# Performance work log

Hardware: AMD Instinct MI355X
Metric: run time of the kernel (lower is better)

Reference implementation:

```python
import jax, jax.numpy as jnp
import numpy as np

DIM = 768
NUM_HEADS = 12
HEAD_DIM = DIM // NUM_HEADS  # 64


def setup_inputs() -> dict:
    key = jax.random.key(0)
    k1, k2, k3, k4 = jax.random.split(key, 4)
    B, N = 2, 2048
    x = jax.random.normal(k1, (B, N, DIM), dtype=jnp.float32)
    att_mask = jnp.ones((B, N), dtype=jnp.int32)
    # learned params (qkv has no bias since qkv_bias=False)
    qkv_w = jax.random.normal(k2, (3 * DIM, DIM), dtype=jnp.float32) * (1.0 / np.sqrt(DIM))
    proj_w = jax.random.normal(k3, (DIM, DIM), dtype=jnp.float32) * (1.0 / np.sqrt(DIM))
    proj_b = jax.random.normal(k4, (DIM,), dtype=jnp.float32) * 0.02
    return {"x": x, "att_mask": att_mask, "qkv_w": qkv_w, "proj_w": proj_w, "proj_b": proj_b}


def reference(x, att_mask, qkv_w, proj_w, proj_b):
    B, N, C = x.shape
    H, Dh = NUM_HEADS, HEAD_DIM
    scale = Dh ** (-0.5)
    # qkv projection: [B,N,3C] -> [3,B,H,N,Dh]
    qkv = jnp.einsum('bnc,oc->bno', x, qkv_w)
    qkv = qkv.reshape(B, N, 3, H, Dh).transpose(2, 0, 3, 1, 4)
    q, k, v = qkv[0], qkv[1], qkv[2]
    q = q * scale
    # full N x N logits (the memory-bound hotspot)
    logit = jnp.einsum('bhnd,bhmd->bhnm', q, k)
    # 2D mask path: [B,N] -> [B,1,1,N], masked_fill(mask==0, -inf)
    mask = att_mask[:, None, None, :]
    logit = jnp.where(mask == 0, -jnp.inf, logit)
    attn = jax.nn.softmax(logit, axis=-1)  # attn_drop is identity (p=0, eval)
    out = jnp.einsum('bhnm,bhmd->bhnd', attn, v)
    out = out.transpose(0, 2, 1, 3).reshape(B, N, H * Dh)
    out = jnp.einsum('bnc,oc->bno', out, proj_w) + proj_b  # proj_drop identity
    return out
```

## Files before the change

### kernel.cpp

```cpp
#include <hip/hip_runtime.h>
#include <hip/hip_bf16.h>
#include <math.h>
#include <cstdint>
#include <cstddef>

typedef __bf16 bf16x8 __attribute__((ext_vector_type(8)));
typedef float  f32x4  __attribute__((ext_vector_type(4)));

#define GLOAD16(g, l) __builtin_amdgcn_global_load_lds( \
    (const __attribute__((address_space(1))) void*)(g),  \
    (__attribute__((address_space(3))) void*)(l), 16, 0, 0)

__device__ __forceinline__ unsigned short f2bf(float f) {
    union { float f; unsigned u; } v; v.f = f;
    unsigned u = v.u;
    u += 0x7fffu + ((u >> 16) & 1u);
    return (unsigned short)(u >> 16);
}

__device__ __forceinline__ unsigned pack_bf16x2(float a, float b) {
    __hip_bfloat162 h = __float22bfloat162_rn(make_float2(a, b));
    return *reinterpret_cast<unsigned*>(&h);
}

__global__ __launch_bounds__(256) void cvt_all(
    const float* __restrict__ x,
    const float* __restrict__ qkvw,
    const float* __restrict__ projw,
    unsigned short* __restrict__ xb,
    unsigned short* __restrict__ wqkv,
    unsigned short* __restrict__ wproj)
{
    const int N1 = 4096 * 768;
    const int N2 = 2304 * 768;
    const int SC = 768 * 768;
    const float C2 = 0.18033688011112042f;
    int i = ((int)blockIdx.x * 256 + (int)threadIdx.x) * 4;

    const float* src;
    unsigned short* dst;
    int j;
    bool sc = false;
    if (i < N1)           { src = x;     dst = xb;    j = i; }
    else if (i < N1 + N2) { j = i - N1;  src = qkvw;  dst = wqkv;  sc = (j < SC); }
    else                  { j = i - N1 - N2; src = projw; dst = wproj; }

    float4 v = *reinterpret_cast<const float4*>(src + j);
    if (sc) { v.x *= C2; v.y *= C2; v.z *= C2; v.w *= C2; }
    uint2 pk;
    pk.x = pack_bf16x2(v.x, v.y);
    pk.y = pack_bf16x2(v.z, v.w);
    *reinterpret_cast<uint2*>(dst + j) = pk;
}

template <int MODE, int MROWS, int NF>
__global__ __launch_bounds__(256) void gemm_bt(
    const unsigned short* __restrict__ A,
    const unsigned short* __restrict__ B,
    unsigned short* __restrict__ Cb,
    unsigned short* __restrict__ Vt,
    float* __restrict__ Cf,
    const float* __restrict__ bias,
    int M, int N, int K)
{
    constexpr int MI = MROWS / 32;
    __shared__ __align__(16) unsigned short Al[2][MROWS * 64];
    __shared__ __align__(16) unsigned short Bl[2][NF * 32 * 64];
    const int bm   = blockIdx.x * MROWS;
    const int bn   = blockIdx.y * (NF * 32);
    const int tid  = (int)threadIdx.x;
    const int wave = tid >> 6;
    const int lane = tid & 63;
    const int wr   = wave >> 1;
    const int wc   = wave & 1;
    const int q    = lane & 15;
    const int g4   = (lane >> 4) * 4;

    f32x4 acc[MI][NF] = {};

    const int srow = lane >> 3;
    const int scol = (lane & 7) * 8;

    auto stage = [&](int buf, int k0) {
#pragma unroll
        for (int i = 0; i < MI; ++i) {
            const int chunk = wave * MI + i;
            GLOAD16(A + (size_t)(bm + chunk * 8 + srow) * K + (k0 + scol),
                    &Al[buf][chunk * 512]);
        }
#pragma unroll
        for (int i = 0; i < NF; ++i) {
            const int chunk = wave * NF + i;
            GLOAD16(B + (size_t)(bn + chunk * 8 + srow) * K + (k0 + scol),
                    &Bl[buf][chunk * 512]);
        }
    };

    stage(0, 0);
    __syncthreads();

    const int nt = K / 64;
    int buf = 0;
    for (int t = 0; t < nt; ++t) {
        if (t + 1 < nt) stage(buf ^ 1, (t + 1) * 64);
#pragma unroll
        for (int kk = 0; kk < 2; ++kk) {
            const int ko = kk * 32 + (lane >> 4) * 8;
            bf16x8 af[MI], bf[NF];
#pragma unroll
            for (int mi = 0; mi < MI; ++mi)
                af[mi] = *(const bf16x8*)&Al[buf][(wr * (MROWS / 2) + mi * 16 + q) * 64 + ko];
#pragma unroll
            for (int ni = 0; ni < NF; ++ni)
                bf[ni] = *(const bf16x8*)&Bl[buf][(wc * 16 * NF + ni * 16 + q) * 64 + ko];
#pragma unroll
            for (int mi = 0; mi < MI; ++mi)
#pragma unroll
                for (int ni = 0; ni < NF; ++ni)
                    acc[mi][ni] = __builtin_amdgcn_mfma_f32_16x16x32_bf16(
                        af[mi], bf[ni], acc[mi][ni], 0, 0, 0);
        }
        __syncthreads();
        buf ^= 1;
    }

#pragma unroll
    for (int mi = 0; mi < MI; ++mi) {
        const int row0 = bm + wr * (MROWS / 2) + mi * 16 + g4;
        if constexpr (MODE == 1) {
#pragma unroll
            for (int ni = 0; ni < NF; ++ni) {
                const int col = bn + wc * 16 * NF + ni * 16 + q;
#pragma unroll
                for (int r = 0; r < 4; ++r)
                    Cf[(size_t)(row0 + r) * N + col] = acc[mi][ni][r] + bias[col];
            }
        } else {
            if (bn < 1536) {
#pragma unroll
                for (int ni = 0; ni < NF; ++ni) {
                    const int col = bn + wc * 16 * NF + ni * 16 + q;
#pragma unroll
                    for (int r = 0; r < 4; ++r)
                        Cb[(size_t)(row0 + r) * 1536 + col] = f2bf(acc[mi][ni][r]);
                }
            } else {
                const int b  = row0 >> 11;
                const int np = row0 & 2047;
#pragma unroll
                for (int ni = 0; ni < NF; ++ni) {
                    const int vcol = bn + wc * 16 * NF + ni * 16 + q - 1536;
                    const int hv = vcol >> 6, d = vcol & 63;
                    uint2 w;
                    w.x = pack_bf16x2(acc[mi][ni][0], acc[mi][ni][1]);
                    w.y = pack_bf16x2(acc[mi][ni][2], acc[mi][ni][3]);
                    *reinterpret_cast<uint2*>(
                        &Vt[((size_t)(b * 12 + hv) * 64 + d) * 2048 + np]) = w;
                }
            }
        }
    }
}

__global__ __launch_bounds__(256, 4) void attn_fwd(
    const unsigned short* __restrict__ qk,
    const unsigned short* __restrict__ vT,
    const int* __restrict__ mask,
    unsigned short* __restrict__ out)
{
    const int NN = 2048, H = 12;
    const int bh = (int)blockIdx.y;
    const int b  = bh / H, h = bh % H;
    const int q0 = (int)blockIdx.x * 64;
    const int tid = (int)threadIdx.x, wave = tid >> 6, lane = tid & 63;
    const int g   = lane >> 4;
    const int q   = lane & 15;
    const int swz = (lane & 7) << 3;

    __shared__ __align__(16) unsigned short Kl[2][64 * 64];
    __shared__ __align__(16) unsigned short Vl[2][64 * 64];
    __shared__ __align__(16) unsigned short Pl[4][16 * 64];

    bool allone;
    {
        const int* mrow = mask + b * NN + lane * 32;
        unsigned mv = 0xFFFFFFFFu;
#pragma unroll
        for (int i = 0; i < 8; ++i) {
            int4 m = *reinterpret_cast<const int4*>(mrow + i * 4);
            mv = min(mv, min(min((unsigned)m.x, (unsigned)m.y),
                             min((unsigned)m.z, (unsigned)m.w)));
        }
        allone = __all(mv != 0u);
    }

    const size_t qrow = (size_t)(b * NN + q0 + wave * 16 + q) * 1536 + h * 64;
    bf16x8 qf[2];
    qf[0] = *reinterpret_cast<const bf16x8*>(&qk[qrow + g * 8]);
    qf[1] = *reinterpret_cast<const bf16x8*>(&qk[qrow + 32 + g * 8]);

    const int srcc = ((lane & 7) ^ (lane >> 3)) * 8;
    const int srow = lane >> 3;
    const char* kg0 = (const char*)(qk + (size_t)(b * NN + wave * 16 + srow) * 1536 + 768 + h * 64 + srcc);
    const char* kg1 = kg0 + (size_t)8 * 1536 * 2;
    const char* vg0 = (const char*)(vT + (size_t)(bh * 64 + wave * 16 + srow) * 2048 + srcc);
    const char* vg1 = vg0 + (size_t)8 * 2048 * 2;

    auto stageK = [&](int buf) {
        GLOAD16(kg0, &Kl[buf][wave * 1024]);
        GLOAD16(kg1, &Kl[buf][wave * 1024 + 512]);
        kg0 += (size_t)64 * 1536 * 2;
        kg1 += (size_t)64 * 1536 * 2;
    };
    auto stageV = [&](int buf) {
        GLOAD16(vg0, &Vl[buf][wave * 1024]);
        GLOAD16(vg1, &Vl[buf][wave * 1024 + 512]);
        vg0 += 128;
        vg1 += 128;
    };

    f32x4 oacc[4] = {};
    float l_i = 0.f;

    stageK(0); stageV(0);
    asm volatile("s_waitcnt vmcnt(0)\n\ts_barrier" ::: "memory");

    int cur = 0;
    for (int it = 0; it < 32; ++it) {
        if (it < 31) { stageV(cur ^ 1); stageK(cur ^ 1); }

        f32x4 s[4] = {};
        __builtin_amdgcn_s_setprio(1);
#pragma unroll
        for (int kk = 0; kk < 2; ++kk) {
            const int ko = kk * 32 + g * 8;
#pragma unroll
            for (int ni = 0; ni < 4; ++ni) {
                bf16x8 kf = *(const bf16x8*)&Kl[cur][(16 * ni + q) * 64 + (ko ^ swz)];
                s[ni] = __builtin_amdgcn_mfma_f32_16x16x32_bf16(kf, qf[kk], s[ni], 0, 0, 0);
            }
        }
        __builtin_amdgcn_s_setprio(0);

        if (!allone) {
#pragma unroll
            for (int ni = 0; ni < 4; ++ni) {
                int4 mr = *reinterpret_cast<const int4*>(
                    &mask[b * NN + it * 64 + 16 * ni + 4 * g]);
                if (mr.x == 0) s[ni][0] = -INFINITY;
                if (mr.y == 0) s[ni][1] = -INFINITY;
                if (mr.z == 0) s[ni][2] = -INFINITY;
                if (mr.w == 0) s[ni][3] = -INFINITY;
            }
        }

        float p[4][4];
#pragma unroll
        for (int ni = 0; ni < 4; ++ni)
#pragma unroll
            for (int r = 0; r < 4; ++r)
                p[ni][r] = __builtin_amdgcn_exp2f(s[ni][r]);
        float rs0 = (p[0][0] + p[0][1]) + (p[0][2] + p[0][3]);
        float rs1 = (p[1][0] + p[1][1]) + (p[1][2] + p[1][3]);
        float rs2 = (p[2][0] + p[2][1]) + (p[2][2] + p[2][3]);
        float rs3 = (p[3][0] + p[3][1]) + (p[3][2] + p[3][3]);
        l_i += (rs0 + rs1) + (rs2 + rs3);

#pragma unroll
        for (int ni = 0; ni < 4; ++ni) {
            uint2 pw;
            pw.x = pack_bf16x2(p[ni][0], p[ni][1]);
            pw.y = pack_bf16x2(p[ni][2], p[ni][3]);
            const int kvb = 16 * ni + 4 * g;
            *reinterpret_cast<uint2*>(&Pl[wave][q * 64 + (kvb ^ ((q & 7) << 3))]) = pw;
        }

        __builtin_amdgcn_s_setprio(1);
#pragma unroll
        for (int kk = 0; kk < 2; ++kk) {
            const int ko = kk * 32 + g * 8;
            bf16x8 pf = *(const bf16x8*)&Pl[wave][q * 64 + (ko ^ ((q & 7) << 3))];
#pragma unroll
            for (int ct = 0; ct < 4; ++ct) {
                bf16x8 vf = *(const bf16x8*)&Vl[cur][(16 * ct + q) * 64 + (ko ^ swz)];
                oacc[ct] = __builtin_amdgcn_mfma_f32_16x16x32_bf16(vf, pf, oacc[ct], 0, 0, 0);
            }
        }
        __builtin_amdgcn_s_setprio(0);

        asm volatile("s_waitcnt vmcnt(0)\n\ts_barrier" ::: "memory");
        cur ^= 1;
    }

    l_i += __shfl_xor(l_i, 16);
    l_i += __shfl_xor(l_i, 32);
    const float inv = 1.0f / l_i;
    const size_t orow = (size_t)(b * NN + q0 + wave * 16 + q) * 768 + h * 64;
#pragma unroll
    for (int ct = 0; ct < 4; ++ct) {
        uint2 ow;
        ow.x = pack_bf16x2(oacc[ct][0] * inv, oacc[ct][1] * inv);
        ow.y = pack_bf16x2(oacc[ct][2] * inv, oacc[ct][3] * inv);
        *reinterpret_cast<uint2*>(&out[orow + 16 * ct + 4 * g]) = ow;
    }
}

extern "C" void kernel_launch(void* const* d_in, const int* in_sizes, int n_in,
                              void* d_out, int out_size, void* d_ws, size_t ws_size,
                              hipStream_t stream)
{
    const float* x      = (const float*)d_in[0];
    const int*   mask   = (const int*)d_in[1];
    const float* qkv_w  = (const float*)d_in[2];
    const float* proj_w = (const float*)d_in[3];
    const float* proj_b = (const float*)d_in[4];
    float* out = (float*)d_out;

    const int BN = 2 * 2048;
    const int C  = 768;
    const int C3 = 2304;

    char* w = (char*)d_ws;
    unsigned short* xb    = (unsigned short*)w; w += (size_t)BN * C    * 2;
    unsigned short* wqkv  = (unsigned short*)w; w += (size_t)C3 * C    * 2;
    unsigned short* wproj = (unsigned short*)w; w += (size_t)C  * C    * 2;
    unsigned short* qk    = (unsigned short*)w; w += (size_t)BN * 1536 * 2;
    unsigned short* vT    = (unsigned short*)w; w += (size_t)24 * 64 * 2048 * 2;
    unsigned short* ao    = (unsigned short*)w;

    {
        const int total = (BN * C + C3 * C + C * C) / 4;
        cvt_all<<<total / 256, 256, 0, stream>>>(x, qkv_w, proj_w, xb, wqkv, wproj);
    }

    gemm_bt<2, 128, 4><<<dim3(BN / 128, C3 / 128), 256, 0, stream>>>(
        xb, wqkv, qk, vT, nullptr, nullptr, BN, C3, C);

    attn_fwd<<<dim3(2048 / 64, 24), 256, 0, stream>>>(qk, vT, mask, ao);

    gemm_bt<1, 64, 2><<<dim3(BN / 64, C / 64), 256, 0, stream>>>(
        ao, wproj, nullptr, nullptr, out, proj_b, BN, C, C);
}
```

Before: 109.1 us.

## Split attention KV tile across waves and reduce partial outputs via LDS

The attention kernel now gives each wave a 16-key slice of each KV tile for all 64 queries, instead of a 16-query slice over all keys. Probabilities stay in registers and feed 16x16x16 MFMAs directly, which removes the per-wave P round-trip through LDS. Each wave keeps a 4x4 accumulator grid and per-query row sums, so partial outputs and sums from the four waves are combined through LDS at the end. The costs are more VGPRs (occupancy bound lowered from 4 to 3), a tree reduction with extra barriers, and twice as many smaller MFMAs in the PV step.

```diff
diff --git a/kernel.cpp b/kernel.cpp
--- a/kernel.cpp
+++ b/kernel.cpp
@@ -5,6 +5,8 @@
 #include <cstddef>
 
 typedef __bf16 bf16x8 __attribute__((ext_vector_type(8)));
+typedef __bf16 bf16x4 __attribute__((ext_vector_type(4)));
+typedef short  s16x4  __attribute__((ext_vector_type(4)));
 typedef float  f32x4  __attribute__((ext_vector_type(4)));
 
 #define GLOAD16(g, l) __builtin_amdgcn_global_load_lds( \
@@ -21,6 +23,19 @@
 __device__ __forceinline__ unsigned pack_bf16x2(float a, float b) {
     __hip_bfloat162 h = __float22bfloat162_rn(make_float2(a, b));
     return *reinterpret_cast<unsigned*>(&h);
+}
+
+__device__ __forceinline__ f32x4 mfma16(bf16x4 a, bf16x4 b, f32x4 c) {
+#if __has_builtin(__builtin_amdgcn_mfma_f32_16x16x16_bf16)
+    return __builtin_amdgcn_mfma_f32_16x16x16_bf16(a, b, c, 0, 0, 0);
+#elif __has_builtin(__builtin_amdgcn_mfma_f32_16x16x16bf16_1k)
+    return __builtin_amdgcn_mfma_f32_16x16x16bf16_1k(
+        __builtin_bit_cast(s16x4, a), __builtin_bit_cast(s16x4, b), c, 0, 0, 0);
+#else
+    asm volatile("v_mfma_f32_16x16x16_bf16 %0, %1, %2, %0"
+                 : "+v"(c) : "v"(a), "v"(b));
+    return c;
+#endif
 }
 
 __global__ __launch_bounds__(256) void cvt_all(
@@ -162,7 +177,7 @@
     }
 }
 
-__global__ __launch_bounds__(256, 4) void attn_fwd(
+__global__ __launch_bounds__(256, 3) void attn_fwd(
     const unsigned short* __restrict__ qk,
     const unsigned short* __restrict__ vT,
     const int* __restrict__ mask,
@@ -175,11 +190,11 @@
     const int tid = (int)threadIdx.x, wave = tid >> 6, lane = tid & 63;
     const int g   = lane >> 4;
     const int q   = lane & 15;
-    const int swz = (lane & 7) << 3;
-
-    __shared__ __align__(16) unsigned short Kl[2][64 * 64];
-    __shared__ __align__(16) unsigned short Vl[2][64 * 64];
-    __shared__ __align__(16) unsigned short Pl[4][16 * 64];
+    const int swz = (q & 7) << 3;
+
+    __shared__ __align__(16) unsigned short LDS[16896];
+    unsigned short* Kl0 = LDS;
+    unsigned short* Vl0 = LDS + 8192;
 
     bool allone;
     {
@@ -194,10 +209,13 @@
         allone = __all(mv != 0u);
     }
 
-    const size_t qrow = (size_t)(b * NN + q0 + wave * 16 + q) * 1536 + h * 64;
-    bf16x8 qf[2];
-    qf[0] = *reinterpret_cast<const bf16x8*>(&qk[qrow + g * 8]);
-    qf[1] = *reinterpret_cast<const bf16x8*>(&qk[qrow + 32 + g * 8]);
+    bf16x8 qf[2][4];
+#pragma unroll
+    for (int kk = 0; kk < 2; ++kk)
+#pragma unroll
+        for (int qt = 0; qt < 4; ++qt)
+            qf[kk][qt] = *reinterpret_cast<const bf16x8*>(
+                &qk[(size_t)(b * NN + q0 + 16 * qt + q) * 1536 + h * 64 + kk * 32 + g * 8]);
 
     const int srcc = ((lane & 7) ^ (lane >> 3)) * 8;
     const int srow = lane >> 3;
@@ -207,20 +225,20 @@
     const char* vg1 = vg0 + (size_t)8 * 2048 * 2;
 
     auto stageK = [&](int buf) {
-        GLOAD16(kg0, &Kl[buf][wave * 1024]);
-        GLOAD16(kg1, &Kl[buf][wave * 1024 + 512]);
+        GLOAD16(kg0, &Kl0[buf * 4096 + wave * 1024]);
+        GLOAD16(kg1, &Kl0[buf * 4096 + wave * 1024 + 512]);
         kg0 += (size_t)64 * 1536 * 2;
         kg1 += (size_t)64 * 1536 * 2;
     };
     auto stageV = [&](int buf) {
-        GLOAD16(vg0, &Vl[buf][wave * 1024]);
-        GLOAD16(vg1, &Vl[buf][wave * 1024 + 512]);
+        GLOAD16(vg0, &Vl0[buf * 4096 + wave * 1024]);
+        GLOAD16(vg1, &Vl0[buf * 4096 + wave * 1024 + 512]);
         vg0 += 128;
         vg1 += 128;
     };
 
-    f32x4 oacc[4] = {};
-    float l_i = 0.f;
+    f32x4 oacc[4][4] = {};
+    float l[4] = {0.f, 0.f, 0.f, 0.f};
 
     stageK(0); stageV(0);
     asm volatile("s_waitcnt vmcnt(0)\n\ts_barrier" ::: "memory");
@@ -233,58 +251,48 @@
         __builtin_amdgcn_s_setprio(1);
 #pragma unroll
         for (int kk = 0; kk < 2; ++kk) {
-            const int ko = kk * 32 + g * 8;
-#pragma unroll
-            for (int ni = 0; ni < 4; ++ni) {
-                bf16x8 kf = *(const bf16x8*)&Kl[cur][(16 * ni + q) * 64 + (ko ^ swz)];
-                s[ni] = __builtin_amdgcn_mfma_f32_16x16x32_bf16(kf, qf[kk], s[ni], 0, 0, 0);
+            bf16x8 kf = *(const bf16x8*)&Kl0[cur * 4096 + (16 * wave + q) * 64
+                                             + ((kk * 32 + g * 8) ^ swz)];
+#pragma unroll
+            for (int qt = 0; qt < 4; ++qt)
+                s[qt] = __builtin_amdgcn_mfma_f32_16x16x32_bf16(kf, qf[kk][qt], s[qt], 0, 0, 0);
+        }
+        __builtin_amdgcn_s_setprio(0);
+
+        if (!allone) {
+            int4 mr = *reinterpret_cast<const int4*>(
+                &mask[b * NN + it * 64 + 16 * wave + 4 * g]);
+#pragma unroll
+            for (int qt = 0; qt < 4; ++qt) {
+                if (mr.x == 0) s[qt][0] = -INFINITY;
+                if (mr.y == 0) s[qt][1] = -INFINITY;
+                if (mr.z == 0) s[qt][2] = -INFINITY;
+                if (mr.w == 0) s[qt][3] = -INFINITY;
             }
         }
-        __builtin_amdgcn_s_setprio(0);
-
-        if (!allone) {
-#pragma unroll
-            for (int ni = 0; ni < 4; ++ni) {
-                int4 mr = *reinterpret_cast<const int4*>(
-                    &mask[b * NN + it * 64 + 16 * ni + 4 * g]);
-                if (mr.x == 0) s[ni][0] = -INFINITY;
-                if (mr.y == 0) s[ni][1] = -INFINITY;
-                if (mr.z == 0) s[ni][2] = -INFINITY;
-                if (mr.w == 0) s[ni][3] = -INFINITY;
-            }
-        }
-
-        float p[4][4];
-#pragma unroll
-        for (int ni = 0; ni < 4; ++ni)
-#pragma unroll
-            for (int r = 0; r < 4; ++r)
-                p[ni][r] = __builtin_amdgcn_exp2f(s[ni][r]);
-        float rs0 = (p[0][0] + p[0][1]) + (p[0][2] + p[0][3]);
-        float rs1 = (p[1][0] + p[1][1]) + (p[1][2] + p[1][3]);
-        float rs2 = (p[2][0] + p[2][1]) + (p[2][2] + p[2][3]);
-        float rs3 = (p[3][0] + p[3][1]) + (p[3][2] + p[3][3]);
-        l_i += (rs0 + rs1) + (rs2 + rs3);
-
-#pragma unroll
-        for (int ni = 0; ni < 4; ++ni) {
-            uint2 pw;
-            pw.x = pack_bf16x2(p[ni][0], p[ni][1]);
-            pw.y = pack_bf16x2(p[ni][2], p[ni][3]);
-            const int kvb = 16 * ni + 4 * g;
-            *reinterpret_cast<uint2*>(&Pl[wave][q * 64 + (kvb ^ ((q & 7) << 3))]) = pw;
+
+        bf16x4 pb[4];
+#pragma unroll
+        for (int qt = 0; qt < 4; ++qt) {
+            float p0 = __builtin_amdgcn_exp2f(s[qt][0]);
+            float p1 = __builtin_amdgcn_exp2f(s[qt][1]);
+            float p2 = __builtin_amdgcn_exp2f(s[qt][2]);
+            float p3 = __builtin_amdgcn_exp2f(s[qt][3]);
+            l[qt] += (p0 + p1) + (p2 + p3);
+            uint2 t;
+            t.x = pack_bf16x2(p0, p1);
+            t.y = pack_bf16x2(p2, p3);
+            pb[qt] = __builtin_bit_cast(bf16x4, t);
         }
 
         __builtin_amdgcn_s_setprio(1);
 #pragma unroll
-        for (int kk = 0; kk < 2; ++kk) {
-            const int ko = kk * 32 + g * 8;
-            bf16x8 pf = *(const bf16x8*)&Pl[wave][q * 64 + (ko ^ ((q & 7) << 3))];
-#pragma unroll
-            for (int ct = 0; ct < 4; ++ct) {
-                bf16x8 vf = *(const bf16x8*)&Vl[cur][(16 * ct + q) * 64 + (ko ^ swz)];
-                oacc[ct] = __builtin_amdgcn_mfma_f32_16x16x32_bf16(vf, pf, oacc[ct], 0, 0, 0);
-            }
+        for (int ct = 0; ct < 4; ++ct) {
+            bf16x4 va = *(const bf16x4*)&Vl0[cur * 4096 + (16 * ct + q) * 64
+                                             + ((16 * wave + 4 * g) ^ swz)];
+#pragma unroll
+            for (int qt = 0; qt < 4; ++qt)
+                oacc[ct][qt] = mfma16(va, pb[qt], oacc[ct][qt]);
         }
         __builtin_amdgcn_s_setprio(0);
 
@@ -292,16 +300,61 @@
         cur ^= 1;
     }
 
-    l_i += __shfl_xor(l_i, 16);
-    l_i += __shfl_xor(l_i, 32);
-    const float inv = 1.0f / l_i;
-    const size_t orow = (size_t)(b * NN + q0 + wave * 16 + q) * 768 + h * 64;
-#pragma unroll
-    for (int ct = 0; ct < 4; ++ct) {
-        uint2 ow;
-        ow.x = pack_bf16x2(oacc[ct][0] * inv, oacc[ct][1] * inv);
-        ow.y = pack_bf16x2(oacc[ct][2] * inv, oacc[ct][3] * inv);
-        *reinterpret_cast<uint2*>(&out[orow + 16 * ct + 4 * g]) = ow;
+#pragma unroll
+    for (int qt = 0; qt < 4; ++qt) {
+        l[qt] += __shfl_xor(l[qt], 16);
+        l[qt] += __shfl_xor(l[qt], 32);
+    }
+    float* lb = (float*)&LDS[16384];
+    float* fb = (float*)&LDS[0];
+    if (g == 0) {
+#pragma unroll
+        for (int qt = 0; qt < 4; ++qt) lb[wave * 64 + qt * 16 + q] = l[qt];
+    }
+    if (wave & 1) {
+        float* dst = fb + (wave >> 1) * 4096;
+#pragma unroll
+        for (int ct = 0; ct < 4; ++ct)
+#pragma unroll
+            for (int qt = 0; qt < 4; ++qt)
+                *reinterpret_cast<f32x4*>(&dst[(ct * 4 + qt) * 256 + lane * 4]) = oacc[ct][qt];
+    }
+    __syncthreads();
+    if (!(wave & 1)) {
+        float* srcp = fb + (wave >> 1) * 4096;
+#pragma unroll
+        for (int ct = 0; ct < 4; ++ct)
+#pragma unroll
+            for (int qt = 0; qt < 4; ++qt)
+                oacc[ct][qt] += *reinterpret_cast<f32x4*>(&srcp[(ct * 4 + qt) * 256 + lane * 4]);
+    }
+    __syncthreads();
+    if (wave == 2) {
+#pragma unroll
+        for (int ct = 0; ct < 4; ++ct)
+#pragma unroll
+            for (int qt = 0; qt < 4; ++qt)
+                *reinterpret_cast<f32x4*>(&fb[(ct * 4 + qt) * 256 + lane * 4]) = oacc[ct][qt];
+    }
+    __syncthreads();
+    if (wave == 0) {
+        float inv[4];
+#pragma unroll
+        for (int qt = 0; qt < 4; ++qt)
+            inv[qt] = 1.0f / (lb[qt * 16 + q] + lb[64 + qt * 16 + q]
+                              + lb[128 + qt * 16 + q] + lb[192 + qt * 16 + q]);
+#pragma unroll
+        for (int ct = 0; ct < 4; ++ct)
+#pragma unroll
+            for (int qt = 0; qt < 4; ++qt) {
+                f32x4 o = oacc[ct][qt]
+                        + *reinterpret_cast<f32x4*>(&fb[(ct * 4 + qt) * 256 + lane * 4]);
+                uint2 ow;
+                ow.x = pack_bf16x2(o[0] * inv[qt], o[1] * inv[qt]);
+                ow.y = pack_bf16x2(o[2] * inv[qt], o[3] * inv[qt]);
+                *reinterpret_cast<uint2*>(
+                    &out[(size_t)(b * NN + q0 + 16 * qt + q) * 768 + h * 64 + 16 * ct + 4 * g]) = ow;
+            }
     }
 }
 
```

New measurement: 110.1 us. About the same (+0.9%).
